# Optimization experiments

Measured on AMD Instinct MI355X. Metric: run time of the kernel, lower is better.

The kernel has to match this reference:

```python
import jax, jax.numpy as jnp
import numpy as np

N = 16384          # replayed items
D_STATE = 2048     # state_dim
D_SEM = 1024       # semantic_dim
S = 4096           # num_semantic_slots
LR = 0.01
DIST_THRESH = 2.0


def setup_inputs() -> dict:
    key = jax.random.key(0)
    k1, k2, k3 = jax.random.split(key, 3)
    replayed_states = jax.random.normal(k1, (N, D_STATE), dtype=jnp.float32)
    replayed_rewards = jax.random.normal(k2, (N,), dtype=jnp.float32)
    # small weight scale so projected content std ~0.05 -> nearest distances
    # straddle the 2.0 threshold and both branches get exercised
    W = jax.random.normal(k3, (D_SEM, D_STATE), dtype=jnp.float32) * (0.05 / np.sqrt(D_STATE))
    b = jnp.zeros((D_SEM,), dtype=jnp.float32)
    semantic_traces = jnp.zeros((S, D_SEM), dtype=jnp.float32)
    trace_strengths = jnp.zeros((S,), dtype=jnp.float32)
    return {
        "replayed_states": replayed_states,
        "replayed_rewards": replayed_rewards,
        "W": W,
        "b": b,
        "semantic_traces": semantic_traces,
        "trace_strengths": trace_strengths,
    }


def _consolidate(content_all, rewards, traces0, strengths0):
    slot_ids = jnp.arange(S, dtype=jnp.int32)

    def step(carry, xs):
        traces, strengths, ptr, num = carry
        content, reward = xs
        reward = jnp.abs(reward)
        valid = jnp.minimum(num, S)
        # euclidean distances to valid slots (invalid -> +inf)
        d = jnp.sqrt(jnp.sum((traces - content[None, :]) ** 2, axis=1))
        d = jnp.where(slot_ids < valid, d, jnp.inf)
        nearest = jnp.argmin(d).astype(jnp.int32)
        nearest_dist = d[nearest]
        do_update = (num > 0) & (nearest_dist < DIST_THRESH)

        # branch A: EMA update of nearest slot
        eff_lr = LR * (1.0 + reward)
        delta = content - traces[nearest]
        traces_u = traces.at[nearest].add(delta * eff_lr)
        strengths_u = strengths.at[nearest].add(1.0)

        # branch B: insert at ring-buffer ptr
        traces_i = traces.at[ptr].set(content)
        strengths_i = strengths.at[ptr].set(1.0)
        ptr_i = (ptr + 1) % S
        num_i = jnp.minimum(num + 1, S)

        traces_n = jnp.where(do_update, traces_u, traces_i)
        strengths_n = jnp.where(do_update, strengths_u, strengths_i)
        ptr_n = jnp.where(do_update, ptr, ptr_i)
        num_n = jnp.where(do_update, num, num_i)
        return (traces_n, strengths_n, ptr_n, num_n), None

    init = (traces0, strengths0, jnp.int32(0), jnp.int32(0))
    (traces, strengths, ptr, num), _ = jax.lax.scan(step, init, (content_all, rewards))
    return traces, strengths, num


def reference(replayed_states, replayed_rewards, W, b, semantic_traces, trace_strengths):
    # projection: nn.Linear -> x @ W.T + b
    content_all = replayed_states @ W.T + b  # (N, D_SEM)
    traces, strengths, num = _consolidate(
        content_all, replayed_rewards, semantic_traces, trace_strengths
    )
    valid_mask = (jnp.arange(S) < jnp.minimum(num, S)).astype(jnp.float32)
    denom = jnp.maximum(valid_mask.sum(), 1.0)
    mean_strength = jnp.where(num > 0, (strengths * valid_mask).sum() / denom, 0.0)
    num_consolidated = jnp.int32(N)  # every item either updates or inserts
    return traces, strengths, num, num_consolidated, mean_strength


if __name__ == "__main__":
    out = reference(**setup_inputs())
    print([getattr(o, "shape", o) for o in out])
```

## Files before the change

### kernel.cpp

```cpp
#include <hip/hip_runtime.h>
#include <cstdint>
#include <cstddef>

#define N_ITEMS 16384
#define D_STATE 2048
#define D_SEM   1024
#define S_SLOTS 4096
#define DTHRESH 2.0f

#define B_ITEMS 256
#define NBLK    (N_ITEMS / B_ITEMS)
#define CHUNK_BLKS 16
#define CHUNK_ITEMS (B_ITEMS * CHUNK_BLKS)

typedef unsigned long long u64;
typedef unsigned int u32;

__global__ __launch_bounds__(256)
void gemm_kernel(const float* __restrict__ A, const float* __restrict__ W,
                 const float* __restrict__ bias, float* __restrict__ C) {
  __shared__ float As[16][68];
  __shared__ float Bs[16][68];
  const int t = threadIdx.x;
  const int ty = t >> 4, tx = t & 15;
  const int i0 = blockIdx.x * 64, j0 = blockIdx.y * 64;
  const int lrow = t >> 2, lcol = (t & 3) << 2;
  float acc[4][4] = {{0.f}};
  const float* ap = A + (size_t)(i0 + lrow) * D_STATE + lcol;
  const float* wp = W + (size_t)(j0 + lrow) * D_STATE + lcol;
  for (int k0 = 0; k0 < D_STATE; k0 += 16) {
    float4 av = *(const float4*)(ap + k0);
    float4 wv = *(const float4*)(wp + k0);
    __syncthreads();
    As[lcol + 0][lrow] = av.x; As[lcol + 1][lrow] = av.y;
    As[lcol + 2][lrow] = av.z; As[lcol + 3][lrow] = av.w;
    Bs[lcol + 0][lrow] = wv.x; Bs[lcol + 1][lrow] = wv.y;
    Bs[lcol + 2][lrow] = wv.z; Bs[lcol + 3][lrow] = wv.w;
    __syncthreads();
#pragma unroll
    for (int kk = 0; kk < 16; kk++) {
      float a[4], b[4];
#pragma unroll
      for (int y = 0; y < 4; y++) a[y] = As[kk][ty * 4 + y];
#pragma unroll
      for (int x = 0; x < 4; x++) b[x] = Bs[kk][tx * 4 + x];
#pragma unroll
      for (int y = 0; y < 4; y++)
#pragma unroll
        for (int x = 0; x < 4; x++) acc[y][x] = fmaf(a[y], b[x], acc[y][x]);
    }
  }
#pragma unroll
  for (int y = 0; y < 4; y++)
#pragma unroll
    for (int x = 0; x < 4; x++) {
      const int col = j0 + tx * 4 + x;
      C[(size_t)(i0 + ty * 4 + y) * D_SEM + col] = acc[y][x] + bias[col];
    }
}

__global__ __launch_bounds__(256)
void gram_kernel(const float* __restrict__ Cc, float* __restrict__ G) {
  const int z = blockIdx.z;
  const float* A = Cc + (size_t)z * B_ITEMS * D_SEM;
  __shared__ float As[16][68];
  __shared__ float Bs[16][68];
  const int t = threadIdx.x;
  const int ty = t >> 4, tx = t & 15;
  const int i0 = blockIdx.x * 64, j0 = blockIdx.y * 64;
  const int lrow = t >> 2, lcol = (t & 3) << 2;
  float acc[4][4] = {{0.f}};
  const float* ap = A + (size_t)(i0 + lrow) * D_SEM + lcol;
  const float* wp = A + (size_t)(j0 + lrow) * D_SEM + lcol;
  for (int k0 = 0; k0 < D_SEM; k0 += 16) {
    float4 av = *(const float4*)(ap + k0);
    float4 wv = *(const float4*)(wp + k0);
    __syncthreads();
    As[lcol + 0][lrow] = av.x; As[lcol + 1][lrow] = av.y;
    As[lcol + 2][lrow] = av.z; As[lcol + 3][lrow] = av.w;
    Bs[lcol + 0][lrow] = wv.x; Bs[lcol + 1][lrow] = wv.y;
    Bs[lcol + 2][lrow] = wv.z; Bs[lcol + 3][lrow] = wv.w;
    __syncthreads();
#pragma unroll
    for (int kk = 0; kk < 16; kk++) {
      float a[4], b[4];
#pragma unroll
      for (int y = 0; y < 4; y++) a[y] = As[kk][ty * 4 + y];
#pragma unroll
      for (int x = 0; x < 4; x++) b[x] = Bs[kk][tx * 4 + x];
#pragma unroll
      for (int y = 0; y < 4; y++)
#pragma unroll
        for (int x = 0; x < 4; x++) acc[y][x] = fmaf(a[y], b[x], acc[y][x]);
    }
  }
  float* Gz = G + (size_t)z * B_ITEMS * B_ITEMS;
#pragma unroll
  for (int y = 0; y < 4; y++)
#pragma unroll
    for (int x = 0; x < 4; x++)
      Gz[(size_t)(i0 + ty * 4 + y) * B_ITEMS + j0 + tx * 4 + x] = acc[y][x];
}

__global__ __launch_bounds__(256)
void pgemm_kernel(const float* __restrict__ A,
                  const float* __restrict__ T,
                  float* __restrict__ P,
                  const int* __restrict__ state) {
  const int limit = min(state[0] + B_ITEMS, S_SLOTS);
  const int j0 = blockIdx.y * 64;
  const int i0 = blockIdx.x * 64;
  const int t = threadIdx.x;
  const int ty = t >> 4, tx = t & 15;
  if (j0 >= limit) {
    const float4 z = {0.f, 0.f, 0.f, 0.f};
    const int col = j0 + tx * 4;
#pragma unroll
    for (int y = 0; y < 4; y++)
      *(float4*)(P + (size_t)(i0 + ty * 4 + y) * S_SLOTS + col) = z;
    return;
  }
  __shared__ float As[16][68];
  __shared__ float Bs[16][68];
  const int lrow = t >> 2, lcol = (t & 3) << 2;
  float acc[4][4] = {{0.f}};
  const float* ap = A + (size_t)(i0 + lrow) * D_SEM + lcol;
  const float* wp = T + (size_t)(j0 + lrow) * D_SEM + lcol;
  for (int k0 = 0; k0 < D_SEM; k0 += 16) {
    float4 av = *(const float4*)(ap + k0);
    float4 wv = *(const float4*)(wp + k0);
    __syncthreads();
    As[lcol + 0][lrow] = av.x; As[lcol + 1][lrow] = av.y;
    As[lcol + 2][lrow] = av.z; As[lcol + 3][lrow] = av.w;
    Bs[lcol + 0][lrow] = wv.x; Bs[lcol + 1][lrow] = wv.y;
    Bs[lcol + 2][lrow] = wv.z; Bs[lcol + 3][lrow] = wv.w;
    __syncthreads();
#pragma unroll
    for (int kk = 0; kk < 16; kk++) {
      float a[4], b[4];
#pragma unroll
      for (int y = 0; y < 4; y++) a[y] = As[kk][ty * 4 + y];
#pragma unroll
      for (int x = 0; x < 4; x++) b[x] = Bs[kk][tx * 4 + x];
#pragma unroll
      for (int y = 0; y < 4; y++)
#pragma unroll
        for (int x = 0; x < 4; x++) acc[y][x] = fmaf(a[y], b[x], acc[y][x]);
    }
  }
#pragma unroll
  for (int y = 0; y < 4; y++)
#pragma unroll
    for (int x = 0; x < 4; x++)
      P[(size_t)(i0 + ty * 4 + y) * S_SLOTS + j0 + tx * 4 + x] = acc[y][x];
}

__global__ __launch_bounds__(256)
void init_kernel(const float* __restrict__ traces0, float* __restrict__ out,
                 float* __restrict__ n_g, int* __restrict__ state) {
  __shared__ float wsum[4];
  const int s = blockIdx.x, t = threadIdx.x;
  const int lane = t & 63, wave = t >> 6;
  float4 v = *(const float4*)(traces0 + (size_t)s * D_SEM + 4 * t);
  *(float4*)(out + (size_t)s * D_SEM + 4 * t) = v;
  float nn = v.x * v.x + v.y * v.y + v.z * v.z + v.w * v.w;
#pragma unroll
  for (int o = 32; o; o >>= 1) nn += __shfl_down(nn, o, 64);
  if (lane == 0) wsum[wave] = nn;
  __syncthreads();
  if (t == 0) n_g[s] = wsum[0] + wsum[1] + wsum[2] + wsum[3];
  if (s == 0 && t == 0) { state[0] = 0; state[1] = 0; }
}

__device__ __forceinline__ float wave_min_f32(float x) {
  int xi = __float_as_int(x), y;
  y = __builtin_amdgcn_update_dpp(xi, xi, 0x111, 0xF, 0xF, false);
  x = fminf(x, __int_as_float(y)); xi = __float_as_int(x);
  y = __builtin_amdgcn_update_dpp(xi, xi, 0x112, 0xF, 0xF, false);
  x = fminf(x, __int_as_float(y)); xi = __float_as_int(x);
  y = __builtin_amdgcn_update_dpp(xi, xi, 0x114, 0xF, 0xF, false);
  x = fminf(x, __int_as_float(y)); xi = __float_as_int(x);
  y = __builtin_amdgcn_update_dpp(xi, xi, 0x118, 0xF, 0xF, false);
  x = fminf(x, __int_as_float(y)); xi = __float_as_int(x);
  y = __builtin_amdgcn_update_dpp(xi, xi, 0x142, 0xA, 0xF, false);
  x = fminf(x, __int_as_float(y)); xi = __float_as_int(x);
  y = __builtin_amdgcn_update_dpp(xi, xi, 0x143, 0xC, 0xF, false);
  x = fminf(x, __int_as_float(y)); xi = __float_as_int(x);
  return __int_as_float(__builtin_amdgcn_readlane(xi, 63));
}

#define CORR_SZ 4352
#define SWZ(s) ((s) + ((s) >> 4))

__global__ __launch_bounds__(256, 1)
void scan_kernel(const float* __restrict__ P, const float* __restrict__ Gb,
                 const float* __restrict__ rewards, const float* __restrict__ n_g,
                 int* __restrict__ state, u64* __restrict__ decs) {
  __shared__ float corr0[CORR_SZ];
  __shared__ float corr1[CORR_SZ];
  __shared__ u64 partials[2][4];
  const int t = threadIdx.x;
  const int lane = t & 63, wave = t >> 6;
  const int s_base = t << 4;
  const int c_base = 17 * t;

  int num = state[0];
  int ptr = state[1];

  for (int s = t; s < CORR_SZ; s += 256) { corr0[s] = 0.f; corr1[s] = 0.f; }

  float n_reg[16];
#pragma unroll
  for (int k = 0; k < 16; k += 4) {
    float4 nv = *(const float4*)(n_g + s_base + k);
    n_reg[k + 0] = (s_base + k + 0 < num) ? nv.x : __uint_as_float(0x7F800000u);
    n_reg[k + 1] = (s_base + k + 1 < num) ? nv.y : __uint_as_float(0x7F800000u);
    n_reg[k + 2] = (s_base + k + 2 < num) ? nv.z : __uint_as_float(0x7F800000u);
    n_reg[k + 3] = (s_base + k + 3 < num) ? nv.w : __uint_as_float(0x7F800000u);
  }
  float alpha_r[16];
#pragma unroll
  for (int k = 0; k < 16; k++) alpha_r[k] = 1.f;

  float p_cur[16], p_n1[16];
#pragma unroll
  for (int k = 0; k < 16; k += 4) {
    float4 v0 = *(const float4*)(P + s_base + k);
    float4 v1 = *(const float4*)(P + (size_t)S_SLOTS + s_base + k);
    p_cur[k] = v0.x; p_cur[k + 1] = v0.y; p_cur[k + 2] = v0.z; p_cur[k + 3] = v0.w;
    p_n1[k]  = v1.x; p_n1[k + 1]  = v1.y; p_n1[k + 2]  = v1.z; p_n1[k + 3]  = v1.w;
  }

  float p_raw_a[16], p_raw_b[16];
  float gc_a, gc_b;
  {
    const float* rp = P + (size_t)2 * S_SLOTS + s_base;
#pragma unroll
    for (int k = 0; k < 16; k += 4) {
      float4 v = *(const float4*)(rp + k);
      p_raw_a[k] = v.x; p_raw_a[k + 1] = v.y; p_raw_a[k + 2] = v.z; p_raw_a[k + 3] = v.w;
    }
    gc_a = Gb[(size_t)2 * B_ITEMS + t];
    gc_b = 0.f;
#pragma unroll
    for (int k = 0; k < 16; k++) p_raw_b[k] = 0.f;
  }

  float gi = Gb[0];
  float ri = rewards[0];
  float g1 = Gb[1];

  int my_cslot = -1; float my_coeff = 0.f;
  u32 my_slot = 0; float my_lr = 0.f;

  __syncthreads();

#define OWNFIX(K, I) { const float nold = n_reg[K]; \
    if (upd) { const float pc = 0.5f * (nold + gi - d2b); \
      n_reg[K] = omr * omr * nold + 2.0f * lr * omr * pc + lr * lr * gi; \
      alpha_r[K] = __fmul_rn(alpha_r[K], omr); \
      if ((I) + 1 < B_ITEMS) p_n1[K] = fmaf(omr, p_n1[K], __fmul_rn(lr, g1)); \
      if ((I) + 2 < B_ITEMS) cv[K] = fmaf(omr, cv[K], __fmul_rn(lr, gf)); \
    } else { n_reg[K] = gi; alpha_r[K] = 0.f; \
      if ((I) + 1 < B_ITEMS) p_n1[K] = g1; \
      if ((I) + 2 < B_ITEMS) cv[K] = gf; } }

#define SCAN_STEP(I, CBUF, RAWC, GCC, RAWN, GCN) { \
     \
    if ((I) + 3 < B_ITEMS) { \
      const float* rp = P + (size_t)((I) + 3) * S_SLOTS + s_base; \
      _Pragma("unroll") \
      for (int k = 0; k < 16; k += 4) { \
        float4 v = *(const float4*)(rp + k); \
        RAWN[k] = v.x; RAWN[k + 1] = v.y; RAWN[k + 2] = v.z; RAWN[k + 3] = v.w; \
      } \
      GCN = Gb[(size_t)((I) + 3) * B_ITEMS + t]; \
    } \
    float gi_n = 0.f, ri_n = 0.f, g1_n = 0.f, gf = 0.f; \
    if ((I) + 1 < B_ITEMS) { \
      gi_n = Gb[(size_t)((I) + 1) * B_ITEMS + (I) + 1]; \
      ri_n = rewards[(I) + 1]; \
      if ((I) + 2 < B_ITEMS) g1_n = Gb[(size_t)((I) + 1) * B_ITEMS + (I) + 2]; \
    } \
    if ((I) + 2 < B_ITEMS) gf = Gb[(size_t)(I) * B_ITEMS + (I) + 2]; \
     \
    if ((I) + 2 < B_ITEMS && my_coeff != 0.f) \
      atomicAdd(&CBUF[SWZ(my_cslot)], __fmul_rn(my_coeff, GCC)); \
     \
    u64 kk[16]; \
    _Pragma("unroll") \
    for (int k = 0; k < 16; k++) { \
      const float v = fmaf(-2.0f, p_cur[k], n_reg[k] + gi); \
      const float d2 = (v > 0.f) ? v : 0.f; \
      kk[k] = ((u64)__float_as_uint(d2) << 32) | (u32)(s_base + k); \
    } \
    _Pragma("unroll") \
    for (int st = 1; st < 16; st <<= 1) \
      _Pragma("unroll") \
      for (int k = 0; k < 16; k += 2 * st) \
        if (kk[k + st] < kk[k]) kk[k] = kk[k + st]; \
    const float d2loc = __uint_as_float((u32)(kk[0] >> 32)); \
    const u32 sloc = (u32)kk[0]; \
     \
    const float dmin = wave_min_f32(d2loc); \
    const u64 bmask = __ballot(d2loc == dmin); \
    const int bl = __ffsll((unsigned long long)bmask) - 1; \
    const u32 swave = (u32)__builtin_amdgcn_readlane((int)sloc, bl); \
    if (lane == 0) \
      partials[(I) & 1][wave] = ((u64)__float_as_uint(dmin) << 32) | swave; \
    asm volatile("s_waitcnt lgkmcnt(0)" ::: "memory"); \
    __builtin_amdgcn_s_barrier(); \
    __builtin_amdgcn_sched_barrier(0); \
     \
    u64 bk = partials[(I) & 1][0]; \
    { u64 v = partials[(I) & 1][1]; if (v < bk) bk = v; \
      v = partials[(I) & 1][2]; if (v < bk) bk = v; \
      v = partials[(I) & 1][3]; if (v < bk) bk = v; } \
    float cv[16]; \
    if ((I) + 2 < B_ITEMS) { \
      _Pragma("unroll") \
      for (int k = 0; k < 16; k++) cv[k] = CBUF[c_base + k]; \
    } else { \
      _Pragma("unroll") \
      for (int k = 0; k < 16; k++) cv[k] = 0.f; \
    } \
    const float d2b = __uint_as_float((u32)(bk >> 32)); \
    const int nslot = (int)(u32)bk; \
    const bool upd = (num > 0) && (d2b < 4.0f); \
    const float lr = __fmul_rn(0.01f, __fadd_rn(1.0f, fabsf(ri))); \
    const int slot = upd ? nslot : ptr; \
    const float omr = 1.0f - lr; \
    if (!upd) { num = min(num + 1, S_SLOTS); ptr = (ptr + 1) & (S_SLOTS - 1); } \
    if ((I) == t) { my_slot = (u32)slot | (upd ? 0x80000000u : 0u); my_lr = lr; } \
    if (my_cslot == slot) my_coeff = upd ? __fmul_rn(my_coeff, omr) : 0.f; \
    if ((I) == t) { my_cslot = slot; my_coeff = upd ? lr : 1.f; } \
     \
    if ((slot >> 4) == t) { \
      switch (slot & 15) { \
        case 0:  OWNFIX(0,  I) break; case 1:  OWNFIX(1,  I) break; \
        case 2:  OWNFIX(2,  I) break; case 3:  OWNFIX(3,  I) break; \
        case 4:  OWNFIX(4,  I) break; case 5:  OWNFIX(5,  I) break; \
        case 6:  OWNFIX(6,  I) break; case 7:  OWNFIX(7,  I) break; \
        case 8:  OWNFIX(8,  I) break; case 9:  OWNFIX(9,  I) break; \
        case 10: OWNFIX(10, I) break; case 11: OWNFIX(11, I) break; \
        case 12: OWNFIX(12, I) break; case 13: OWNFIX(13, I) break; \
        case 14: OWNFIX(14, I) break; default: OWNFIX(15, I) break; \
      } \
    } \
     \
    _Pragma("unroll") \
    for (int k = 0; k < 16; k++) p_cur[k] = p_n1[k]; \
    if ((I) + 2 < B_ITEMS) { \
      _Pragma("unroll") \
      for (int k = 0; k < 16; k++) { \
        p_n1[k] = fmaf(alpha_r[k], RAWC[k], cv[k]); \
        CBUF[c_base + k] = 0.f; \
      } \
    } \
    gi = gi_n; ri = ri_n; g1 = g1_n; \
  }

  for (int i = 0; i < B_ITEMS; i += 2) {
    SCAN_STEP(i,     corr0, p_raw_a, gc_a, p_raw_b, gc_b)
    SCAN_STEP(i + 1, corr1, p_raw_b, gc_b, p_raw_a, gc_a)
  }
#undef SCAN_STEP
#undef OWNFIX

  if (t == 0) { state[0] = num; state[1] = ptr; }
  decs[t] = ((u64)__float_as_uint(my_lr) << 32) | (u64)my_slot;
}

__global__ __launch_bounds__(256)
void apply_kernel(const float* __restrict__ content,
                  const u64* __restrict__ decs,
                  float* __restrict__ traces,
                  float* __restrict__ n_g) {
  __shared__ u32 aslot[B_ITEMS];
  __shared__ float alr[B_ITEMS];
  __shared__ float betas[B_ITEMS];
  __shared__ int notowner;
  __shared__ float wsum[4];
  const int t = threadIdx.x, j = blockIdx.x;
  const int lane = t & 63, wave = t >> 6;
  const u64 d = decs[t];
  aslot[t] = (u32)(d & 0xFFFFFFFFull);
  alr[t] = __uint_as_float((u32)(d >> 32));
  if (t == 0) notowner = 0;
  __syncthreads();
  const u32 myslot = aslot[j] & 0x7FFFFFFFu;
  if (t > j && (aslot[t] & 0x7FFFFFFFu) == myslot) notowner = 1;
  __syncthreads();
  if (notowner) return;

  float alpha = 1.f, beta = 0.f;
  for (int k = 0; k < B_ITEMS; k++) {
    const u32 a = aslot[k];
    if ((a & 0x7FFFFFFFu) == myslot) {
      const float lr = alr[k];
      if (a & 0x80000000u) {
        const float om = 1.f - lr;
        alpha *= om; beta *= om;
        if (t == k) beta += lr;
      } else {
        alpha = 0.f; beta = (t == k) ? 1.f : 0.f;
      }
    }
  }
  betas[t] = beta;
  __syncthreads();

  float4 v = *(const float4*)(traces + (size_t)myslot * D_SEM + 4 * t);
  v.x *= alpha; v.y *= alpha; v.z *= alpha; v.w *= alpha;
  for (int k = 0; k < B_ITEMS; k++) {
    if ((aslot[k] & 0x7FFFFFFFu) == myslot) {
      const float bk = betas[k];
      const float4 c = *(const float4*)(content + (size_t)k * D_SEM + 4 * t);
      v.x = fmaf(bk, c.x, v.x); v.y = fmaf(bk, c.y, v.y);
      v.z = fmaf(bk, c.z, v.z); v.w = fmaf(bk, c.w, v.w);
    }
  }
  *(float4*)(traces + (size_t)myslot * D_SEM + 4 * t) = v;
  float nn = v.x * v.x + v.y * v.y + v.z * v.z + v.w * v.w;
#pragma unroll
  for (int o = 32; o; o >>= 1) nn += __shfl_down(nn, o, 64);
  if (lane == 0) wsum[wave] = nn;
  __syncthreads();
  if (t == 0) n_g[myslot] = wsum[0] + wsum[1] + wsum[2] + wsum[3];
}

__global__ __launch_bounds__(256)
void finalize_kernel(const float* __restrict__ strengths0,
                     const u64* __restrict__ decs,
                     const int* __restrict__ state, float* __restrict__ out) {
  __shared__ int last_ins[S_SLOTS];
  __shared__ int cnt[S_SLOTS];
  __shared__ float wsum[4];
  const int t = threadIdx.x, lane = t & 63, wave = t >> 6;
  for (int s = t; s < S_SLOTS; s += 256) { last_ins[s] = -1; cnt[s] = 0; }
  __syncthreads();
  for (int k = t; k < N_ITEMS; k += 256) {
    const u32 dd = (u32)(decs[k] & 0xFFFFFFFFull);
    if (!(dd & 0x80000000u)) atomicMax(&last_ins[(int)dd], k);
  }
  __syncthreads();
  for (int k = t; k < N_ITEMS; k += 256) {
    const u32 dd = (u32)(decs[k] & 0xFFFFFFFFull);
    const int slot = (int)(dd & 0x7FFFFFFFu);
    if ((dd & 0x80000000u) && k > last_ins[slot]) atomicAdd(&cnt[slot], 1);
  }
  __syncthreads();
  const int num = state[0];
  float* outs = out + (size_t)S_SLOTS * D_SEM;
  float lsum = 0.f;
  for (int s = t; s < S_SLOTS; s += 256) {
    const float base = (last_ins[s] >= 0) ? 1.f : strengths0[s];
    const float v = base + (float)cnt[s];
    outs[s] = v;
    if (s < num) lsum += v;
  }
#pragma unroll
  for (int o = 32; o; o >>= 1) lsum += __shfl_down(lsum, o, 64);
  if (lane == 0) wsum[wave] = lsum;
  __syncthreads();
  if (t == 0) {
    const float total = wsum[0] + wsum[1] + wsum[2] + wsum[3];
    float denom = (float)num;
    if (denom < 1.f) denom = 1.f;
    outs[S_SLOTS + 0] = (float)num;
    outs[S_SLOTS + 1] = (float)N_ITEMS;
    outs[S_SLOTS + 2] = (num > 0) ? (total / denom) : 0.f;
  }
}

extern "C" void kernel_launch(void* const* d_in, const int* in_sizes, int n_in,
                              void* d_out, int out_size, void* d_ws, size_t ws_size,
                              hipStream_t stream) {
  const float* states  = (const float*)d_in[0];
  const float* rewards = (const float*)d_in[1];
  const float* W       = (const float*)d_in[2];
  const float* bias    = (const float*)d_in[3];
  const float* traces0 = (const float*)d_in[4];
  const float* str0    = (const float*)d_in[5];
  float* out = (float*)d_out;

  char* p = (char*)d_ws;
  float* cbuf = (float*)p;                 p += (size_t)CHUNK_ITEMS * D_SEM * 4;
  float* P    = (float*)p;                 p += (size_t)B_ITEMS * S_SLOTS * 4;
  float* Gb   = (float*)p;                 p += (size_t)CHUNK_BLKS * B_ITEMS * B_ITEMS * 4;
  float* n_g  = (float*)p;                 p += (size_t)S_SLOTS * 4;
  u64*   decs = (u64*)p;                   p += (size_t)N_ITEMS * 8;
  int*   state = (int*)p;

  init_kernel<<<S_SLOTS, 256, 0, stream>>>(traces0, out, n_g, state);

  for (int c = 0; c < N_ITEMS / CHUNK_ITEMS; c++) {
    gemm_kernel<<<dim3(CHUNK_ITEMS / 64, D_SEM / 64), 256, 0, stream>>>(
        states + (size_t)c * CHUNK_ITEMS * D_STATE, W, bias, cbuf);
    gram_kernel<<<dim3(4, 4, CHUNK_BLKS), 256, 0, stream>>>(cbuf, Gb);
    for (int bb = 0; bb < CHUNK_BLKS; bb++) {
      const int b = c * CHUNK_BLKS + bb;
      const float* cblk = cbuf + (size_t)bb * B_ITEMS * D_SEM;
      const float* Gblk = Gb + (size_t)bb * B_ITEMS * B_ITEMS;
      pgemm_kernel<<<dim3(4, S_SLOTS / 64), 256, 0, stream>>>(cblk, out, P, state);
      scan_kernel<<<1, 256, 0, stream>>>(P, Gblk, rewards + (size_t)b * B_ITEMS,
                                         n_g, state, decs + (size_t)b * B_ITEMS);
      apply_kernel<<<B_ITEMS, 256, 0, stream>>>(cblk, decs + (size_t)b * B_ITEMS,
                                                out, n_g);
    }
  }
  finalize_kernel<<<1, 256, 0, stream>>>(str0, decs, state, out);
}
```

Measured before the change: 32.26 ms.

## Shorten scan lookahead pipeline from two items to one and simplify argmin

Cuts the sequential scan's software pipeline depth. The next item's inner products are now built at the end of each step, so the extra p_n1 register array and its owner-fix bookkeeping go away. The per-thread argmin no longer uses a 64-bit key tree reduction; it takes an fminf reduction plus a first-index search. This lowers register pressure and per-step instruction count, but exposes more latency because the corrections must be ready one step later.

```diff
diff --git a/kernel.cpp b/kernel.cpp
--- a/kernel.cpp
+++ b/kernel.cpp
@@ -222,33 +222,30 @@
 #pragma unroll
   for (int k = 0; k < 16; k++) alpha_r[k] = 1.f;
 
-  float p_cur[16], p_n1[16];
+  float p_cur[16];
 #pragma unroll
   for (int k = 0; k < 16; k += 4) {
     float4 v0 = *(const float4*)(P + s_base + k);
-    float4 v1 = *(const float4*)(P + (size_t)S_SLOTS + s_base + k);
     p_cur[k] = v0.x; p_cur[k + 1] = v0.y; p_cur[k + 2] = v0.z; p_cur[k + 3] = v0.w;
-    p_n1[k]  = v1.x; p_n1[k + 1]  = v1.y; p_n1[k + 2]  = v1.z; p_n1[k + 3]  = v1.w;
-  }
-
-  float p_raw_a[16], p_raw_b[16];
+  }
+
+  float raw_a[16], raw_b[16];
   float gc_a, gc_b;
   {
-    const float* rp = P + (size_t)2 * S_SLOTS + s_base;
+    const float* rp = P + (size_t)S_SLOTS + s_base;
 #pragma unroll
     for (int k = 0; k < 16; k += 4) {
       float4 v = *(const float4*)(rp + k);
-      p_raw_a[k] = v.x; p_raw_a[k + 1] = v.y; p_raw_a[k + 2] = v.z; p_raw_a[k + 3] = v.w;
-    }
-    gc_a = Gb[(size_t)2 * B_ITEMS + t];
+      raw_a[k] = v.x; raw_a[k + 1] = v.y; raw_a[k + 2] = v.z; raw_a[k + 3] = v.w;
+    }
+    gc_a = Gb[(size_t)B_ITEMS + t];
     gc_b = 0.f;
 #pragma unroll
-    for (int k = 0; k < 16; k++) p_raw_b[k] = 0.f;
+    for (int k = 0; k < 16; k++) raw_b[k] = 0.f;
   }
 
   float gi = Gb[0];
   float ri = rewards[0];
-  float g1 = Gb[1];
 
   int my_cslot = -1; float my_coeff = 0.f;
   u32 my_slot = 0; float my_lr = 0.f;
@@ -256,54 +253,50 @@
   __syncthreads();
 
 #define OWNFIX(K, I) { const float nold = n_reg[K]; \
-    if (upd) { const float pc = 0.5f * (nold + gi - d2b); \
-      n_reg[K] = omr * omr * nold + 2.0f * lr * omr * pc + lr * lr * gi; \
+    if (upd) { \
+      n_reg[K] = omr * omr * nold + 2.0f * lr * omr * p_cur[K] + lr * lr * gi; \
       alpha_r[K] = __fmul_rn(alpha_r[K], omr); \
-      if ((I) + 1 < B_ITEMS) p_n1[K] = fmaf(omr, p_n1[K], __fmul_rn(lr, g1)); \
-      if ((I) + 2 < B_ITEMS) cv[K] = fmaf(omr, cv[K], __fmul_rn(lr, gf)); \
+      if ((I) + 1 < B_ITEMS) cv[K] = fmaf(omr, cv[K], __fmul_rn(lr, g1)); \
     } else { n_reg[K] = gi; alpha_r[K] = 0.f; \
-      if ((I) + 1 < B_ITEMS) p_n1[K] = g1; \
-      if ((I) + 2 < B_ITEMS) cv[K] = gf; } }
+      if ((I) + 1 < B_ITEMS) cv[K] = g1; } }
 
 #define SCAN_STEP(I, CBUF, RAWC, GCC, RAWN, GCN) { \
      \
-    if ((I) + 3 < B_ITEMS) { \
-      const float* rp = P + (size_t)((I) + 3) * S_SLOTS + s_base; \
+    if ((I) + 2 < B_ITEMS) { \
+      const float* rp = P + (size_t)((I) + 2) * S_SLOTS + s_base; \
       _Pragma("unroll") \
       for (int k = 0; k < 16; k += 4) { \
         float4 v = *(const float4*)(rp + k); \
         RAWN[k] = v.x; RAWN[k + 1] = v.y; RAWN[k + 2] = v.z; RAWN[k + 3] = v.w; \
       } \
-      GCN = Gb[(size_t)((I) + 3) * B_ITEMS + t]; \
+      GCN = Gb[(size_t)((I) + 2) * B_ITEMS + t]; \
     } \
-    float gi_n = 0.f, ri_n = 0.f, g1_n = 0.f, gf = 0.f; \
+    float gi_n = 0.f, ri_n = 0.f, g1 = 0.f; \
     if ((I) + 1 < B_ITEMS) { \
       gi_n = Gb[(size_t)((I) + 1) * B_ITEMS + (I) + 1]; \
       ri_n = rewards[(I) + 1]; \
-      if ((I) + 2 < B_ITEMS) g1_n = Gb[(size_t)((I) + 1) * B_ITEMS + (I) + 2]; \
+      g1   = Gb[(size_t)(I) * B_ITEMS + (I) + 1]; \
     } \
-    if ((I) + 2 < B_ITEMS) gf = Gb[(size_t)(I) * B_ITEMS + (I) + 2]; \
-     \
-    if ((I) + 2 < B_ITEMS && my_coeff != 0.f) \
+     \
+    if ((I) + 1 < B_ITEMS && my_coeff != 0.f) \
       atomicAdd(&CBUF[SWZ(my_cslot)], __fmul_rn(my_coeff, GCC)); \
      \
-    u64 kk[16]; \
+    float d2[16]; \
     _Pragma("unroll") \
     for (int k = 0; k < 16; k++) { \
       const float v = fmaf(-2.0f, p_cur[k], n_reg[k] + gi); \
-      const float d2 = (v > 0.f) ? v : 0.f; \
-      kk[k] = ((u64)__float_as_uint(d2) << 32) | (u32)(s_base + k); \
+      d2[k] = (v > 0.f) ? v : 0.f; \
     } \
+    float dloc = d2[0]; \
     _Pragma("unroll") \
-    for (int st = 1; st < 16; st <<= 1) \
-      _Pragma("unroll") \
-      for (int k = 0; k < 16; k += 2 * st) \
-        if (kk[k + st] < kk[k]) kk[k] = kk[k + st]; \
-    const float d2loc = __uint_as_float((u32)(kk[0] >> 32)); \
-    const u32 sloc = (u32)kk[0]; \
-     \
-    const float dmin = wave_min_f32(d2loc); \
-    const u64 bmask = __ballot(d2loc == dmin); \
+    for (int k = 1; k < 16; k++) dloc = fminf(dloc, d2[k]); \
+    u32 iloc = 0; \
+    _Pragma("unroll") \
+    for (int k = 15; k >= 1; k--) if (d2[k] == dloc) iloc = (u32)k; \
+    const u32 sloc = (u32)s_base + iloc; \
+     \
+    const float dmin = wave_min_f32(dloc); \
+    const u64 bmask = __ballot(dloc == dmin); \
     const int bl = __ffsll((unsigned long long)bmask) - 1; \
     const u32 swave = (u32)__builtin_amdgcn_readlane((int)sloc, bl); \
     if (lane == 0) \
@@ -317,7 +310,7 @@
       v = partials[(I) & 1][2]; if (v < bk) bk = v; \
       v = partials[(I) & 1][3]; if (v < bk) bk = v; } \
     float cv[16]; \
-    if ((I) + 2 < B_ITEMS) { \
+    if ((I) + 1 < B_ITEMS) { \
       _Pragma("unroll") \
       for (int k = 0; k < 16; k++) cv[k] = CBUF[c_base + k]; \
     } else { \
@@ -348,21 +341,19 @@
       } \
     } \
      \
-    _Pragma("unroll") \
-    for (int k = 0; k < 16; k++) p_cur[k] = p_n1[k]; \
-    if ((I) + 2 < B_ITEMS) { \
+    if ((I) + 1 < B_ITEMS) { \
       _Pragma("unroll") \
       for (int k = 0; k < 16; k++) { \
-        p_n1[k] = fmaf(alpha_r[k], RAWC[k], cv[k]); \
+        p_cur[k] = fmaf(alpha_r[k], RAWC[k], cv[k]); \
         CBUF[c_base + k] = 0.f; \
       } \
     } \
-    gi = gi_n; ri = ri_n; g1 = g1_n; \
+    gi = gi_n; ri = ri_n; \
   }
 
   for (int i = 0; i < B_ITEMS; i += 2) {
-    SCAN_STEP(i,     corr0, p_raw_a, gc_a, p_raw_b, gc_b)
-    SCAN_STEP(i + 1, corr1, p_raw_b, gc_b, p_raw_a, gc_a)
+    SCAN_STEP(i,     corr0, raw_a, gc_a, raw_b, gc_b)
+    SCAN_STEP(i + 1, corr1, raw_b, gc_b, raw_a, gc_a)
   }
 #undef SCAN_STEP
 #undef OWNFIX
```

New measurement: 33.38 ms. +3.5%, slower.
